# Kernel tuning notes

Measured on AMD Instinct MI355X. Metric: run time of the kernel, lower is better.

## Reference

```python
import jax, jax.numpy as jnp
import numpy as np

B = 262144
N = 256      # mode size of every TT core
R = 8        # tt_rank
D = 8        # number of cores = 7 state dims + 1 action dim
STD = 0.001


def setup_inputs() -> dict:
    key = jax.random.key(0)
    ks = jax.random.split(key, D + 2)
    inp = {}
    # TT cores: G0 (1,N,R), G1..G6 (R,N,R), G7 (R,N,1)
    inp["G0"] = jax.random.normal(ks[0], (1, N, R), dtype=jnp.float32) * STD
    for k in range(1, D - 1):
        inp[f"G{k}"] = jax.random.normal(ks[k], (R, N, R), dtype=jnp.float32) * STD
    inp[f"G{D-1}"] = jax.random.normal(ks[D - 1], (R, N, 1), dtype=jnp.float32) * STD
    inp["states"] = jax.random.randint(ks[D], (B, 7), 0, N, dtype=jnp.int32)
    inp["actions"] = jax.random.randint(ks[D + 1], (B,), 0, N, dtype=jnp.int32)
    return inp


def reference(G0, G1, G2, G3, G4, G5, G6, G7, states, actions):
    # mode 'q_sa': concat state indices with action index -> (B, D)
    idx = jnp.concatenate(
        [states.reshape(-1, 7), actions.reshape(-1, 1)], axis=1
    )
    cores = [G0, G1, G2, G3, G4, G5, G6, G7]
    # t3f.gather_nd: chain of per-core gathers + tiny batched matmuls.
    # vec starts as the gathered slice of the first core: (B, R)
    vec = cores[0][0, idx[:, 0], :]
    for k in range(1, D):
        # gather slices along mode axis: (B, r_prev, r_next)
        sl = jnp.transpose(jnp.take(cores[k], idx[:, k], axis=1), (1, 0, 2))
        vec = jnp.einsum("br,brs->bs", vec, sl)
    # final vec has shape (B, 1); Q(s,a) values per batch element
    return vec[:, 0]
```

## Files before the change

### kernel.cpp

```cpp
#include <hip/hip_runtime.h>


#define NN 256
#define RR 8
#define NR 2048
#define U67_OFF 524288
#define GT_OFF  1048576

__device__ __forceinline__ unsigned short f2bf_rne(float f) {
    unsigned int u = __float_as_uint(f);
    u += 0x7FFFu + ((u >> 16) & 1u);
    return (unsigned short)(u >> 16);
}

__device__ __forceinline__ uint4 pack8bf(const float* a) {
    return make_uint4(
        f2bf_rne(a[0]) | ((unsigned int)f2bf_rne(a[1]) << 16),
        f2bf_rne(a[2]) | ((unsigned int)f2bf_rne(a[3]) << 16),
        f2bf_rne(a[4]) | ((unsigned int)f2bf_rne(a[5]) << 16),
        f2bf_rne(a[6]) | ((unsigned int)f2bf_rne(a[7]) << 16));
}

__global__ __launch_bounds__(256) void build_tables(
    const float* __restrict__ G0, const float* __restrict__ G1,
    const float* __restrict__ G2, const float* __restrict__ G3,
    const float* __restrict__ G4, const float* __restrict__ G5,
    const float* __restrict__ G6, const float* __restrict__ G7,
    unsigned short* __restrict__ wsb) {
    const int t = threadIdx.x;
    const int bid = blockIdx.x;

    if (bid < NN) {
        const int n0 = bid, n1 = t;
        float acc[RR] = {0.f,0.f,0.f,0.f,0.f,0.f,0.f,0.f};
#pragma unroll
        for (int r = 0; r < RR; ++r) {
            float ar = G0[n0 * RR + r];
            const float4* p = (const float4*)(G1 + r * NR + n1 * RR);
            float4 x = p[0], y = p[1];
            acc[0] += ar * x.x; acc[1] += ar * x.y;
            acc[2] += ar * x.z; acc[3] += ar * x.w;
            acc[4] += ar * y.x; acc[5] += ar * y.y;
            acc[6] += ar * y.z; acc[7] += ar * y.w;
        }
        *(uint4*)(wsb + n0 * 2048 + n1 * 8) = pack8bf(acc);
    } else if (bid < 2 * NN) {
        const int n6 = bid - NN, n7 = t;
        float g7v[RR];
#pragma unroll
        for (int s = 0; s < RR; ++s) g7v[s] = G7[s * NN + n7];
        float u[RR];
#pragma unroll
        for (int r = 0; r < RR; ++r) {
            float acc = 0.f;
#pragma unroll
            for (int s = 0; s < RR; ++s)
                acc += G6[r * NR + n6 * RR + s] * g7v[s];
            u[r] = acc;
        }
        *(uint4*)(wsb + U67_OFF + n6 * 2048 + n7 * 8) = pack8bf(u);
    } else {
        const int q = bid - 2 * NN;
        const int k = q >> 3;
        const int chunk = q & 7;
        const float* __restrict__ Gk =
            (k == 0) ? G2 : (k == 1) ? G3 : (k == 2) ? G4 : G5;
        const int n = chunk * 32 + (t >> 3);
        const int r = t & 7;
        const float4* src = (const float4*)(Gk + r * NR + n * RR);
        float4 x = src[0], y = src[1];
        float a[8] = {x.x, x.y, x.z, x.w, y.x, y.y, y.z, y.w};
        *(uint4*)(wsb + GT_OFF + k * 16384 + n * 64 + r * 8) = pack8bf(a);
    }
}

#define BF2F_LO(u) __uint_as_float((u) << 16)
#define BF2F_HI(u) __uint_as_float((u) & 0xFFFF0000u)

#define BSTAGE(koff, nidx)                                                  \
    do {                                                                    \
        const uint4* mp =                                                   \
            (const uint4*)(wsb + GT_OFF + (koff)*16384 + (nidx)*64);        \
        float nv0 = 0.f, nv1 = 0.f, nv2 = 0.f, nv3 = 0.f;                   \
        float nv4 = 0.f, nv5 = 0.f, nv6 = 0.f, nv7 = 0.f;                   \
        _Pragma("unroll") for (int r = 0; r < 8; ++r) {                     \
            uint4 u = mp[r];                                                \
            float vr = v[r];                                                \
            nv0 += vr * BF2F_LO(u.x); nv1 += vr * BF2F_HI(u.x);             \
            nv2 += vr * BF2F_LO(u.y); nv3 += vr * BF2F_HI(u.y);             \
            nv4 += vr * BF2F_LO(u.z); nv5 += vr * BF2F_HI(u.z);             \
            nv6 += vr * BF2F_LO(u.w); nv7 += vr * BF2F_HI(u.w);             \
        }                                                                   \
        v[0] = nv0; v[1] = nv1; v[2] = nv2; v[3] = nv3;                     \
        v[4] = nv4; v[5] = nv5; v[6] = nv6; v[7] = nv7;                     \
    } while (0)

__global__ __launch_bounds__(256) void tt_gather(
    const unsigned short* __restrict__ wsb,
    const int* __restrict__ states, const int* __restrict__ actions,
    float* __restrict__ out, int B) {
    __shared__ int ibuf[NN * 7];

    const int t = threadIdx.x;
    const int b = blockIdx.x * 256 + t;

    {
        const int* gsrc = states + (size_t)blockIdx.x * 256 * 7;
        const int lim = B * 7 - blockIdx.x * 256 * 7;
#pragma unroll
        for (int k = 0; k < 7; ++k) {
            int j = t + (k << 8);
            if (j < lim) ibuf[j] = gsrc[j];
        }
    }
    __syncthreads();

    const bool active = (b < B);
    const int* row = ibuf + t * 7;
    const int s0 = row[0] & 255;
    const int s1 = row[1] & 255;
    const int s2 = row[2] & 255;
    const int s3 = row[3] & 255;
    const int s4 = row[4] & 255;
    const int s5 = row[5] & 255;
    const int s6 = row[6] & 255;
    const int a7 = actions[active ? b : 0] & 255;

    float v[8];
    {
        uint4 u = *(const uint4*)(wsb + s0 * 2048 + s1 * 8);
        v[0] = BF2F_LO(u.x); v[1] = BF2F_HI(u.x);
        v[2] = BF2F_LO(u.y); v[3] = BF2F_HI(u.y);
        v[4] = BF2F_LO(u.z); v[5] = BF2F_HI(u.z);
        v[6] = BF2F_LO(u.w); v[7] = BF2F_HI(u.w);
    }

    BSTAGE(0, s2);
    BSTAGE(1, s3);
    BSTAGE(2, s4);
    BSTAGE(3, s5);

    float q;
    {
        uint4 u = *(const uint4*)(wsb + U67_OFF + s6 * 2048 + a7 * 8);
        q = v[0] * BF2F_LO(u.x) + v[1] * BF2F_HI(u.x)
          + v[2] * BF2F_LO(u.y) + v[3] * BF2F_HI(u.y)
          + v[4] * BF2F_LO(u.z) + v[5] * BF2F_HI(u.z)
          + v[6] * BF2F_LO(u.w) + v[7] * BF2F_HI(u.w);
    }
    if (active) out[b] = q;
}

extern "C" void kernel_launch(void* const* d_in, const int* in_sizes, int n_in,
                              void* d_out, int out_size, void* d_ws, size_t ws_size,
                              hipStream_t stream) {
    const float* G0 = (const float*)d_in[0];
    const float* G1 = (const float*)d_in[1];
    const float* G2 = (const float*)d_in[2];
    const float* G3 = (const float*)d_in[3];
    const float* G4 = (const float*)d_in[4];
    const float* G5 = (const float*)d_in[5];
    const float* G6 = (const float*)d_in[6];
    const float* G7 = (const float*)d_in[7];
    const int* states  = (const int*)d_in[8];
    const int* actions = (const int*)d_in[9];
    float* out = (float*)d_out;
    int B = in_sizes[9];

    unsigned short* wsb = (unsigned short*)d_ws;

    hipLaunchKernelGGL(build_tables, dim3(2 * NN + 32), dim3(256), 0, stream,
                       G0, G1, G2, G3, G4, G5, G6, G7, wsb);

    hipLaunchKernelGGL(tt_gather, dim3((B + 255) / 256), dim3(256), 0, stream,
                       wsb, states, actions, out, B);
}
```

Baseline: 102.6 us.

## Precompute pairwise G2·G3 and G4·G5 product tables to shorten per-sample chain

```diff
diff --git a/kernel.cpp b/kernel.cpp
--- a/kernel.cpp
+++ b/kernel.cpp
@@ -5,7 +5,8 @@
 #define RR 8
 #define NR 2048
 #define U67_OFF 524288
-#define GT_OFF  1048576
+#define T23_OFF 1048576
+#define T45_OFF 5242880
 
 __device__ __forceinline__ unsigned short f2bf_rne(float f) {
     unsigned int u = __float_as_uint(f);
@@ -27,6 +28,7 @@
     const float* __restrict__ G4, const float* __restrict__ G5,
     const float* __restrict__ G6, const float* __restrict__ G7,
     unsigned short* __restrict__ wsb) {
+    __shared__ float Ash[64];
     const int t = threadIdx.x;
     const int bid = blockIdx.x;
 
@@ -61,39 +63,45 @@
         *(uint4*)(wsb + U67_OFF + n6 * 2048 + n7 * 8) = pack8bf(u);
     } else {
         const int q = bid - 2 * NN;
-        const int k = q >> 3;
-        const int chunk = q & 7;
-        const float* __restrict__ Gk =
-            (k == 0) ? G2 : (k == 1) ? G3 : (k == 2) ? G4 : G5;
-        const int n = chunk * 32 + (t >> 3);
-        const int r = t & 7;
-        const float4* src = (const float4*)(Gk + r * NR + n * RR);
-        float4 x = src[0], y = src[1];
-        float a[8] = {x.x, x.y, x.z, x.w, y.x, y.y, y.z, y.w};
-        *(uint4*)(wsb + GT_OFF + k * 16384 + n * 64 + r * 8) = pack8bf(a);
+        const int isT45 = q >> 8;
+        const int n2 = q & 255;
+        const float* __restrict__ A = isT45 ? G4 : G2;
+        const float* __restrict__ Bm = isT45 ? G5 : G3;
+        unsigned short* __restrict__ dst =
+            wsb + (isT45 ? T45_OFF : T23_OFF);
+
+        if (t < 16) {
+            const int r = t >> 1, h = t & 1;
+            *(float4*)(Ash + r * 8 + h * 4) =
+                *(const float4*)(A + r * NR + n2 * RR + h * 4);
+        }
+        __syncthreads();
+
+        const int n3 = t;
+        float acc[64];
+#pragma unroll
+        for (int i = 0; i < 64; ++i) acc[i] = 0.f;
+#pragma unroll
+        for (int m = 0; m < 8; ++m) {
+            const float4* bp = (const float4*)(Bm + m * NR + n3 * RR);
+            float4 b0 = bp[0], b1 = bp[1];
+#pragma unroll
+            for (int r = 0; r < 8; ++r) {
+                float a = Ash[r * 8 + m];
+                acc[r*8+0] += a * b0.x; acc[r*8+1] += a * b0.y;
+                acc[r*8+2] += a * b0.z; acc[r*8+3] += a * b0.w;
+                acc[r*8+4] += a * b1.x; acc[r*8+5] += a * b1.y;
+                acc[r*8+6] += a * b1.z; acc[r*8+7] += a * b1.w;
+            }
+        }
+        uint4* o = (uint4*)(dst + ((n2 << 8) + n3) * 64);
+#pragma unroll
+        for (int r = 0; r < 8; ++r) o[r] = pack8bf(acc + r * 8);
     }
 }
 
 #define BF2F_LO(u) __uint_as_float((u) << 16)
 #define BF2F_HI(u) __uint_as_float((u) & 0xFFFF0000u)
-
-#define BSTAGE(koff, nidx)                                                  \
-    do {                                                                    \
-        const uint4* mp =                                                   \
-            (const uint4*)(wsb + GT_OFF + (koff)*16384 + (nidx)*64);        \
-        float nv0 = 0.f, nv1 = 0.f, nv2 = 0.f, nv3 = 0.f;                   \
-        float nv4 = 0.f, nv5 = 0.f, nv6 = 0.f, nv7 = 0.f;                   \
-        _Pragma("unroll") for (int r = 0; r < 8; ++r) {                     \
-            uint4 u = mp[r];                                                \
-            float vr = v[r];                                                \
-            nv0 += vr * BF2F_LO(u.x); nv1 += vr * BF2F_HI(u.x);             \
-            nv2 += vr * BF2F_LO(u.y); nv3 += vr * BF2F_HI(u.y);             \
-            nv4 += vr * BF2F_LO(u.z); nv5 += vr * BF2F_HI(u.z);             \
-            nv6 += vr * BF2F_LO(u.w); nv7 += vr * BF2F_HI(u.w);             \
-        }                                                                   \
-        v[0] = nv0; v[1] = nv1; v[2] = nv2; v[3] = nv3;                     \
-        v[4] = nv4; v[5] = nv5; v[6] = nv6; v[7] = nv7;                     \
-    } while (0)
 
 __global__ __launch_bounds__(256) void tt_gather(
     const unsigned short* __restrict__ wsb,
@@ -126,28 +134,53 @@
     const int s6 = row[6] & 255;
     const int a7 = actions[active ? b : 0] & 255;
 
+    const uint4* p01 = (const uint4*)(wsb + s0 * 2048 + s1 * 8);
+    const uint4* p23 = (const uint4*)(wsb + T23_OFF + ((s2 << 8) + s3) * 64);
+    const uint4* p45 = (const uint4*)(wsb + T45_OFF + ((s4 << 8) + s5) * 64);
+    const uint4* p67 = (const uint4*)(wsb + U67_OFF + s6 * 2048 + a7 * 8);
+
+    uint4 uv = *p01;
+    uint4 m[8], w[8];
+#pragma unroll
+    for (int r = 0; r < 8; ++r) m[r] = p23[r];
+#pragma unroll
+    for (int r = 0; r < 8; ++r) w[r] = p45[r];
+    uint4 ue = *p67;
+
     float v[8];
-    {
-        uint4 u = *(const uint4*)(wsb + s0 * 2048 + s1 * 8);
-        v[0] = BF2F_LO(u.x); v[1] = BF2F_HI(u.x);
-        v[2] = BF2F_LO(u.y); v[3] = BF2F_HI(u.y);
-        v[4] = BF2F_LO(u.z); v[5] = BF2F_HI(u.z);
-        v[6] = BF2F_LO(u.w); v[7] = BF2F_HI(u.w);
-    }
-
-    BSTAGE(0, s2);
-    BSTAGE(1, s3);
-    BSTAGE(2, s4);
-    BSTAGE(3, s5);
-
-    float q;
-    {
-        uint4 u = *(const uint4*)(wsb + U67_OFF + s6 * 2048 + a7 * 8);
-        q = v[0] * BF2F_LO(u.x) + v[1] * BF2F_HI(u.x)
-          + v[2] * BF2F_LO(u.y) + v[3] * BF2F_HI(u.y)
-          + v[4] * BF2F_LO(u.z) + v[5] * BF2F_HI(u.z)
-          + v[6] * BF2F_LO(u.w) + v[7] * BF2F_HI(u.w);
-    }
+    v[0] = BF2F_LO(uv.x); v[1] = BF2F_HI(uv.x);
+    v[2] = BF2F_LO(uv.y); v[3] = BF2F_HI(uv.y);
+    v[4] = BF2F_LO(uv.z); v[5] = BF2F_HI(uv.z);
+    v[6] = BF2F_LO(uv.w); v[7] = BF2F_HI(uv.w);
+
+    float nv[8];
+#pragma unroll
+    for (int i = 0; i < 8; ++i) nv[i] = 0.f;
+#pragma unroll
+    for (int r = 0; r < 8; ++r) {
+        float vr = v[r];
+        nv[0] += vr * BF2F_LO(m[r].x); nv[1] += vr * BF2F_HI(m[r].x);
+        nv[2] += vr * BF2F_LO(m[r].y); nv[3] += vr * BF2F_HI(m[r].y);
+        nv[4] += vr * BF2F_LO(m[r].z); nv[5] += vr * BF2F_HI(m[r].z);
+        nv[6] += vr * BF2F_LO(m[r].w); nv[7] += vr * BF2F_HI(m[r].w);
+    }
+
+    float fv[8];
+#pragma unroll
+    for (int i = 0; i < 8; ++i) fv[i] = 0.f;
+#pragma unroll
+    for (int r = 0; r < 8; ++r) {
+        float vr = nv[r];
+        fv[0] += vr * BF2F_LO(w[r].x); fv[1] += vr * BF2F_HI(w[r].x);
+        fv[2] += vr * BF2F_LO(w[r].y); fv[3] += vr * BF2F_HI(w[r].y);
+        fv[4] += vr * BF2F_LO(w[r].z); fv[5] += vr * BF2F_HI(w[r].z);
+        fv[6] += vr * BF2F_LO(w[r].w); fv[7] += vr * BF2F_HI(w[r].w);
+    }
+
+    float q = fv[0] * BF2F_LO(ue.x) + fv[1] * BF2F_HI(ue.x)
+            + fv[2] * BF2F_LO(ue.y) + fv[3] * BF2F_HI(ue.y)
+            + fv[4] * BF2F_LO(ue.z) + fv[5] * BF2F_HI(ue.z)
+            + fv[6] * BF2F_LO(ue.w) + fv[7] * BF2F_HI(ue.w);
     if (active) out[b] = q;
 }
 
@@ -169,7 +202,7 @@
 
     unsigned short* wsb = (unsigned short*)d_ws;
 
-    hipLaunchKernelGGL(build_tables, dim3(2 * NN + 32), dim3(256), 0, stream,
+    hipLaunchKernelGGL(build_tables, dim3(2 * NN + 512), dim3(256), 0, stream,
                        G0, G1, G2, G3, G4, G5, G6, G7, wsb);
 
     hipLaunchKernelGGL(tt_gather, dim3((B + 255) / 256), dim3(256), 0, stream,
```

After: 104.3 us. Within noise of the previous version (+1.7%).

## Stage middle TT cores in LDS with transposed layout, use 1024-thread blocks

Applied to the files above, without the earlier changes.

```diff
diff --git a/kernel.cpp b/kernel.cpp
--- a/kernel.cpp
+++ b/kernel.cpp
@@ -6,6 +6,7 @@
 #define NR 2048
 #define U67_OFF 524288
 #define GT_OFF  1048576
+#define GT_CORE 16384
 
 __device__ __forceinline__ unsigned short f2bf_rne(float f) {
     unsigned int u = __float_as_uint(f);
@@ -70,84 +71,102 @@
         const float4* src = (const float4*)(Gk + r * NR + n * RR);
         float4 x = src[0], y = src[1];
         float a[8] = {x.x, x.y, x.z, x.w, y.x, y.y, y.z, y.w};
-        *(uint4*)(wsb + GT_OFF + k * 16384 + n * 64 + r * 8) = pack8bf(a);
+        *(uint4*)(wsb + GT_OFF + k * GT_CORE + r * 2048 + n * 8) = pack8bf(a);
     }
 }
 
 #define BF2F_LO(u) __uint_as_float((u) << 16)
 #define BF2F_HI(u) __uint_as_float((u) & 0xFFFF0000u)
 
-#define BSTAGE(koff, nidx)                                                  \
+#define LSTAGE(k, nidx)                                                     \
     do {                                                                    \
-        const uint4* mp =                                                   \
-            (const uint4*)(wsb + GT_OFF + (koff)*16384 + (nidx)*64);        \
-        float nv0 = 0.f, nv1 = 0.f, nv2 = 0.f, nv3 = 0.f;                   \
-        float nv4 = 0.f, nv5 = 0.f, nv6 = 0.f, nv7 = 0.f;                   \
-        _Pragma("unroll") for (int r = 0; r < 8; ++r) {                     \
-            uint4 u = mp[r];                                                \
-            float vr = v[r];                                                \
-            nv0 += vr * BF2F_LO(u.x); nv1 += vr * BF2F_HI(u.x);             \
-            nv2 += vr * BF2F_LO(u.y); nv3 += vr * BF2F_HI(u.y);             \
-            nv4 += vr * BF2F_LO(u.z); nv5 += vr * BF2F_HI(u.z);             \
-            nv6 += vr * BF2F_LO(u.w); nv7 += vr * BF2F_HI(u.w);             \
-        }                                                                   \
+        const uint4* mp = l4 + (k) * 2048 + (nidx);                         \
+        uint4 r0 = mp[0],    r1 = mp[256],  r2 = mp[512],  r3 = mp[768];    \
+        uint4 r4 = mp[1024], r5 = mp[1280], r6 = mp[1536], r7 = mp[1792];   \
+        float nv0, nv1, nv2, nv3, nv4, nv5, nv6, nv7;                       \
+        nv0  = v[0] * BF2F_LO(r0.x); nv1  = v[0] * BF2F_HI(r0.x);           \
+        nv2  = v[0] * BF2F_LO(r0.y); nv3  = v[0] * BF2F_HI(r0.y);           \
+        nv4  = v[0] * BF2F_LO(r0.z); nv5  = v[0] * BF2F_HI(r0.z);           \
+        nv6  = v[0] * BF2F_LO(r0.w); nv7  = v[0] * BF2F_HI(r0.w);           \
+        nv0 += v[1] * BF2F_LO(r1.x); nv1 += v[1] * BF2F_HI(r1.x);           \
+        nv2 += v[1] * BF2F_LO(r1.y); nv3 += v[1] * BF2F_HI(r1.y);           \
+        nv4 += v[1] * BF2F_LO(r1.z); nv5 += v[1] * BF2F_HI(r1.z);           \
+        nv6 += v[1] * BF2F_LO(r1.w); nv7 += v[1] * BF2F_HI(r1.w);           \
+        nv0 += v[2] * BF2F_LO(r2.x); nv1 += v[2] * BF2F_HI(r2.x);           \
+        nv2 += v[2] * BF2F_LO(r2.y); nv3 += v[2] * BF2F_HI(r2.y);           \
+        nv4 += v[2] * BF2F_LO(r2.z); nv5 += v[2] * BF2F_HI(r2.z);           \
+        nv6 += v[2] * BF2F_LO(r2.w); nv7 += v[2] * BF2F_HI(r2.w);           \
+        nv0 += v[3] * BF2F_LO(r3.x); nv1 += v[3] * BF2F_HI(r3.x);           \
+        nv2 += v[3] * BF2F_LO(r3.y); nv3 += v[3] * BF2F_HI(r3.y);           \
+        nv4 += v[3] * BF2F_LO(r3.z); nv5 += v[3] * BF2F_HI(r3.z);           \
+        nv6 += v[3] * BF2F_LO(r3.w); nv7 += v[3] * BF2F_HI(r3.w);           \
+        nv0 += v[4] * BF2F_LO(r4.x); nv1 += v[4] * BF2F_HI(r4.x);           \
+        nv2 += v[4] * BF2F_LO(r4.y); nv3 += v[4] * BF2F_HI(r4.y);           \
+        nv4 += v[4] * BF2F_LO(r4.z); nv5 += v[4] * BF2F_HI(r4.z);           \
+        nv6 += v[4] * BF2F_LO(r4.w); nv7 += v[4] * BF2F_HI(r4.w);           \
+        nv0 += v[5] * BF2F_LO(r5.x); nv1 += v[5] * BF2F_HI(r5.x);           \
+        nv2 += v[5] * BF2F_LO(r5.y); nv3 += v[5] * BF2F_HI(r5.y);           \
+        nv4 += v[5] * BF2F_LO(r5.z); nv5 += v[5] * BF2F_HI(r5.z);           \
+        nv6 += v[5] * BF2F_LO(r5.w); nv7 += v[5] * BF2F_HI(r5.w);           \
+        nv0 += v[6] * BF2F_LO(r6.x); nv1 += v[6] * BF2F_HI(r6.x);           \
+        nv2 += v[6] * BF2F_LO(r6.y); nv3 += v[6] * BF2F_HI(r6.y);           \
+        nv4 += v[6] * BF2F_LO(r6.z); nv5 += v[6] * BF2F_HI(r6.z);           \
+        nv6 += v[6] * BF2F_LO(r6.w); nv7 += v[6] * BF2F_HI(r6.w);           \
+        nv0 += v[7] * BF2F_LO(r7.x); nv1 += v[7] * BF2F_HI(r7.x);           \
+        nv2 += v[7] * BF2F_LO(r7.y); nv3 += v[7] * BF2F_HI(r7.y);           \
+        nv4 += v[7] * BF2F_LO(r7.z); nv5 += v[7] * BF2F_HI(r7.z);           \
+        nv6 += v[7] * BF2F_LO(r7.w); nv7 += v[7] * BF2F_HI(r7.w);           \
         v[0] = nv0; v[1] = nv1; v[2] = nv2; v[3] = nv3;                     \
         v[4] = nv4; v[5] = nv5; v[6] = nv6; v[7] = nv7;                     \
     } while (0)
 
-__global__ __launch_bounds__(256) void tt_gather(
+__global__ __launch_bounds__(1024) void tt_gather(
     const unsigned short* __restrict__ wsb,
     const int* __restrict__ states, const int* __restrict__ actions,
     float* __restrict__ out, int B) {
-    __shared__ int ibuf[NN * 7];
+    __shared__ unsigned short lut[4 * GT_CORE];
 
     const int t = threadIdx.x;
-    const int b = blockIdx.x * 256 + t;
 
     {
-        const int* gsrc = states + (size_t)blockIdx.x * 256 * 7;
-        const int lim = B * 7 - blockIdx.x * 256 * 7;
+        const uint4* src = (const uint4*)(wsb + GT_OFF);
+        uint4* dst = (uint4*)lut;
 #pragma unroll
-        for (int k = 0; k < 7; ++k) {
-            int j = t + (k << 8);
-            if (j < lim) ibuf[j] = gsrc[j];
-        }
+        for (int i = 0; i < 8; ++i) dst[t + (i << 10)] = src[t + (i << 10)];
     }
     __syncthreads();
 
+    const int b = blockIdx.x * 1024 + t;
     const bool active = (b < B);
-    const int* row = ibuf + t * 7;
-    const int s0 = row[0] & 255;
-    const int s1 = row[1] & 255;
-    const int s2 = row[2] & 255;
-    const int s3 = row[3] & 255;
-    const int s4 = row[4] & 255;
-    const int s5 = row[5] & 255;
-    const int s6 = row[6] & 255;
+    const int base = active ? b * 7 : 0;
+    const int s0 = states[base + 0] & 255;
+    const int s1 = states[base + 1] & 255;
+    const int s2 = states[base + 2] & 255;
+    const int s3 = states[base + 3] & 255;
+    const int s4 = states[base + 4] & 255;
+    const int s5 = states[base + 5] & 255;
+    const int s6 = states[base + 6] & 255;
     const int a7 = actions[active ? b : 0] & 255;
 
+    const uint4 uv = *(const uint4*)(wsb + s0 * 2048 + s1 * 8);
+    const uint4 ue = *(const uint4*)(wsb + U67_OFF + s6 * 2048 + a7 * 8);
+
     float v[8];
-    {
-        uint4 u = *(const uint4*)(wsb + s0 * 2048 + s1 * 8);
-        v[0] = BF2F_LO(u.x); v[1] = BF2F_HI(u.x);
-        v[2] = BF2F_LO(u.y); v[3] = BF2F_HI(u.y);
-        v[4] = BF2F_LO(u.z); v[5] = BF2F_HI(u.z);
-        v[6] = BF2F_LO(u.w); v[7] = BF2F_HI(u.w);
-    }
+    v[0] = BF2F_LO(uv.x); v[1] = BF2F_HI(uv.x);
+    v[2] = BF2F_LO(uv.y); v[3] = BF2F_HI(uv.y);
+    v[4] = BF2F_LO(uv.z); v[5] = BF2F_HI(uv.z);
+    v[6] = BF2F_LO(uv.w); v[7] = BF2F_HI(uv.w);
 
-    BSTAGE(0, s2);
-    BSTAGE(1, s3);
-    BSTAGE(2, s4);
-    BSTAGE(3, s5);
+    const uint4* l4 = (const uint4*)lut;
+    LSTAGE(0, s2);
+    LSTAGE(1, s3);
+    LSTAGE(2, s4);
+    LSTAGE(3, s5);
 
-    float q;
-    {
-        uint4 u = *(const uint4*)(wsb + U67_OFF + s6 * 2048 + a7 * 8);
-        q = v[0] * BF2F_LO(u.x) + v[1] * BF2F_HI(u.x)
-          + v[2] * BF2F_LO(u.y) + v[3] * BF2F_HI(u.y)
-          + v[4] * BF2F_LO(u.z) + v[5] * BF2F_HI(u.z)
-          + v[6] * BF2F_LO(u.w) + v[7] * BF2F_HI(u.w);
-    }
+    float q = v[0] * BF2F_LO(ue.x) + v[1] * BF2F_HI(ue.x)
+            + v[2] * BF2F_LO(ue.y) + v[3] * BF2F_HI(ue.y)
+            + v[4] * BF2F_LO(ue.z) + v[5] * BF2F_HI(ue.z)
+            + v[6] * BF2F_LO(ue.w) + v[7] * BF2F_HI(ue.w);
     if (active) out[b] = q;
 }
 
@@ -172,6 +191,6 @@
     hipLaunchKernelGGL(build_tables, dim3(2 * NN + 32), dim3(256), 0, stream,
                        G0, G1, G2, G3, G4, G5, G6, G7, wsb);
 
-    hipLaunchKernelGGL(tt_gather, dim3((B + 255) / 256), dim3(256), 0, stream,
+    hipLaunchKernelGGL(tt_gather, dim3((B + 1023) / 1024), dim3(1024), 0, stream,
                        wsb, states, actions, out, B);
 }
```

Measured after the change: 121.9 us. +18.8%, slower.
